# Kernel optimization log

Hardware: AMD Instinct MI355X
Metric: run time of the kernel (lower is better)

The kernel has to match this reference:

```python
import jax, jax.numpy as jnp
import numpy as np

CX, CY, FX, FY = 334.081, 169.808, 460.585, 460.268
EPS = 1e-07
T_ITER = 1000
MIN_POINTS = 5000
H, W, B = 360, 640, 2


def _point_cloud(depth_img):
    # depth_img: [C,H,W]; channel 2 if C==3 else channel 0
    depth = depth_img[2] if depth_img.shape[0] == 3 else depth_img[0]
    rows, cols = depth.shape
    c = jnp.arange(cols, dtype=depth.dtype)[None, :]
    r = jnp.arange(rows, dtype=depth.dtype)[:, None]
    valid = (depth > 0) & (depth < 65535)
    nanv = jnp.float32(jnp.nan)
    z = jnp.where(valid, depth / 1000.0, nanv)
    x = jnp.where(valid, z * (c - CX) / FX, nanv)
    y = jnp.where(valid, z * (r - CY) / FY, nanv)
    pcd = jnp.stack([x.ravel(), y.ravel(), z.ravel()], axis=1)  # [N,3]
    return pcd, valid.ravel()


def setup_inputs() -> dict:
    key = jax.random.key(0)
    k1, k2 = jax.random.split(key)
    fake = jax.random.uniform(k1, (B, 1, H, W), dtype=jnp.float32)
    real = jax.random.uniform(k2, (B, 1, H, W), dtype=jnp.float32)
    return {"fake": fake, "real": real, "epoch": 5, "show_image": 0}


def _forward(fake, real, epoch):
    real_pcd, vr = _point_cloud(real[0])
    fake_pcd, vf = _point_cloud(fake[0])
    real_pcd = real_pcd * 1000.0
    fake_pcd = fake_pcd * 1000.0
    # pcd[pcd==0] = eps  (NaN==0 is False, NaNs preserved)
    real_pcd = jnp.where(real_pcd == 0, EPS, real_pcd)
    fake_pcd = jnp.where(fake_pcd == 0, EPS, fake_pcd)

    # combined validity mask (real-valid then fake-valid filtering chain)
    m = vr & vf
    cnt = jnp.maximum(jnp.sum(m), 1)

    def sel(v, fill):
        return jnp.where(m, v, fill)

    def mrmse(a, b):
        d = sel(a, 0.0) - sel(b, 0.0)
        return jnp.sqrt(jnp.sum(d * d) / cnt)

    lossX = mrmse(real_pcd[:, 0], fake_pcd[:, 0])
    lossY = mrmse(real_pcd[:, 1], fake_pcd[:, 1])
    lossZ = mrmse(real_pcd[:, 2], fake_pcd[:, 2])
    dlog = jnp.log(jnp.abs(sel(real_pcd[:, 2], 1.0))) - jnp.log(jnp.abs(sel(fake_pcd[:, 2], 1.0)))
    RMSE_log = 10000.0 * jnp.sqrt(jnp.sum(jnp.where(m, dlog * dlog, 0.0)) / cnt)
    loss17 = RMSE_log * jnp.abs(10.0 * (3.0 - jnp.exp(lossX) - jnp.exp(lossY) - jnp.exp(lossZ)))

    # ---- batched RANSAC plane fit on normalized fake cloud ----
    nan_cloud = jnp.where(jnp.isnan(fake_pcd), 0.0, fake_pcd)
    pts = nan_cloud / jnp.max(nan_cloud)  # [N,3]
    N = pts.shape[0]
    thresh = jnp.maximum(jnp.float32(0.025 - 0.001 * epoch), jnp.float32(0.005))

    rkey = jax.random.key(42)
    idx = jax.random.randint(rkey, (T_ITER, 3), 0, N)  # 3 sample points per trial
    p = pts[idx]  # [T,3,3]
    vA = p[:, 1] - p[:, 0]
    vB = p[:, 2] - p[:, 0]
    nrm = jnp.cross(vA, vB)
    nrm = nrm / jnp.linalg.norm(nrm, axis=1, keepdims=True)  # unit normals [T,3]
    kk = -jnp.sum(nrm * p[:, 1], axis=1)  # plane offsets [T]
    dist = pts @ nrm.T + kk[None, :]  # [N,T], |n|=1 so no extra divide
    inl = jnp.abs(dist) <= thresh  # [N,T]
    counts = jnp.sum(inl, axis=0)  # [T]
    # keep first trial with strictly-largest count among counts > minPoints
    score = jnp.where(counts > MIN_POINTS, counts, -1)
    best = jnp.argmax(score)
    a, b, c, d = nrm[best, 0], nrm[best, 1], nrm[best, 2], kk[best]
    inlier_mask = inl[:, best]  # [N]

    # translation/rotation were built via torch.tensor(...) -> detached in torch
    trans = jax.lax.stop_gradient(jnp.stack([jnp.zeros(()), jnp.zeros(()), d / c]))
    n2 = a * a + b * b + c * c
    cos_t = c / jnp.sqrt(n2)
    sin_t = jnp.sqrt((a * a + b * b) / n2)
    sab = jnp.sqrt(a * a + b * b)
    u1 = b / sab
    u2 = -a / sab
    R = jnp.stack([
        jnp.stack([cos_t + u1 * u1 * (1 - cos_t), u1 * u2 * (1 - cos_t), u2 * sin_t]),
        jnp.stack([u1 * u2 * (1 - cos_t), cos_t + u2 * u2 * (1 - cos_t), -u1 * sin_t]),
        jnp.stack([-u2 * sin_t, u1 * sin_t, cos_t]),
    ])
    Rt = jax.lax.stop_gradient(R).T  # torch transposes before matmul

    plane_pts = pts + trans
    zc = (plane_pts @ Rt)[:, 2]  # rotated z for all points; inliers selected by mask
    icnt = jnp.maximum(jnp.sum(inlier_mask), 1)
    zmax = jnp.max(jnp.where(inlier_mask, zc, -jnp.inf))
    zmin = jnp.min(jnp.where(inlier_mask, zc, jnp.inf))
    below = jnp.sum(jnp.where(inlier_mask, jnp.abs(zc - zmax), 0.0)) / icnt
    above = jnp.sum(jnp.where(inlier_mask, jnp.abs(zc - zmin), 0.0)) / icnt
    above = jnp.where(above == 0, jnp.float32(1e-07), above)
    plane_mean_dist_grad = 1000.0 * (above + below)

    loss_curv = loss17 + plane_mean_dist_grad
    delta = jnp.stack([RMSE_log, lossX, lossY, lossZ, plane_mean_dist_grad, loss17])
    return delta, loss_curv


def reference(fake, real, epoch, show_image):
    del show_image  # unused in the loss math
    return _forward(fake, real, epoch)
```

## Files before the change

kernel.cpp:

```cpp
#include <hip/hip_runtime.h>

namespace {

typedef float v2f __attribute__((ext_vector_type(2)));

constexpr int kW = 640;
constexpr unsigned kSpan = 230400u;
constexpr int kB1 = 900;
constexpr int kB3 = 1800;
constexpr int kPPB3 = 128;
constexpr int kChunk = 113;
constexpr int kB5 = 900;

constexpr size_t kOffMaxv    = 0;
constexpr size_t kOffL17     = 8;
constexpr size_t kOffSel     = 16;
constexpr size_t kOffPlanes  = 512;
constexpr size_t kOffSP      = 512 + 16384;
constexpr size_t kOffZP      = 60416;
constexpr size_t kOffPartial = 90112;
constexpr size_t kOffPts     = 2097152;

__device__ __forceinline__ unsigned rotl32(unsigned v, int r) {
  return (v << r) | (v >> (32 - r));
}

__device__ __forceinline__ void threefry(unsigned c0, unsigned c1,
                                         unsigned& o0, unsigned& o1) {
  const unsigned ks0 = 0u, ks1 = 42u, ks2 = 0x1BD11BDAu ^ 0u ^ 42u;
  unsigned x0 = c0 + ks0, x1 = c1 + ks1;
#define TFR(r) { x0 += x1; x1 = rotl32(x1, (r)); x1 ^= x0; }
  TFR(13) TFR(15) TFR(26) TFR(6)
  x0 += ks1; x1 += ks2 + 1u;
  TFR(17) TFR(29) TFR(16) TFR(24)
  x0 += ks2; x1 += ks0 + 2u;
  TFR(13) TFR(15) TFR(26) TFR(6)
  x0 += ks0; x1 += ks1 + 3u;
  TFR(17) TFR(29) TFR(16) TFR(24)
  x0 += ks1; x1 += ks2 + 4u;
  TFR(13) TFR(15) TFR(26) TFR(6)
  x0 += ks2; x1 += ks0 + 5u;
#undef TFR
  o0 = x0; o1 = x1;
}

__device__ __forceinline__ void pix_coords(float d, int row, int col, bool& valid,
                                           float& x, float& y, float& z) {
  valid = (d > 0.0f) && (d < 65535.0f);
  float z0 = d / 1000.0f;
  float x0 = z0 * ((float)col - 334.081f) / 460.585f;
  float y0 = z0 * ((float)row - 169.808f) / 460.268f;
  x = x0 * 1000.0f;
  y = y0 * 1000.0f;
  z = z0 * 1000.0f;
  if (x == 0.0f) x = 1e-7f;
  if (y == 0.0f) y = 1e-7f;
  if (z == 0.0f) z = 1e-7f;
}

__device__ __forceinline__ void make_pt(float d, int row, int col, float maxv,
                                        float& x, float& y, float& z) {
  bool v; float a, b, c;
  pix_coords(d, row, col, v, a, b, c);
  x = (v ? a : 0.f) / maxv;
  y = (v ? b : 0.f) / maxv;
  z = (v ? c : 0.f) / maxv;
}

__device__ __forceinline__ float get_thresh(int ep) {
  return (float)fmax(0.025 - 0.001 * (double)ep, 0.005);
}

__global__ __launch_bounds__(256) void k_stats(const float* __restrict__ fake,
                                               const float* __restrict__ real,
                                               char* __restrict__ ws) {
  int* maxvBits = (int*)(ws + kOffMaxv);
  double* sp = (double*)(ws + kOffSP);
  float4* ptsraw = (float4*)(ws + kOffPts);

  const int b = blockIdx.x, t = threadIdx.x;
  const int lane = t & 63, wid = t >> 6;

  __shared__ double sD0[4], sD1[4], sD2[4], sD3[4];
  __shared__ int sI0[4];
  __shared__ float sF0[4];

  int i = b * 256 + t;
  int row = i / kW, col = i - row * kW;
  bool vr, vf; float rx, ry, rz, fx, fy, fz;
  pix_coords(real[i], row, col, vr, rx, ry, rz);
  pix_coords(fake[i], row, col, vf, fx, fy, fz);
  ptsraw[i] = make_float4(vf ? fx : 0.f, vf ? fy : 0.f, vf ? fz : 0.f, 0.f);
  double dx2 = 0, dy2 = 0, dz2 = 0, dl2 = 0; int cc = 0;
  if (vr && vf) {
    float ddx = rx - fx, ddy = ry - fy, ddz = rz - fz;
    dx2 = (double)ddx * (double)ddx;
    dy2 = (double)ddy * (double)ddy;
    dz2 = (double)ddz * (double)ddz;
    double dl = log(fabs((double)rz)) - log(fabs((double)fz));
    dl2 = dl * dl;
    cc = 1;
  }
  float mx = vf ? fmaxf(fmaxf(fx, fy), fz) : 0.0f;
  for (int o = 32; o; o >>= 1) {
    dx2 += __shfl_down(dx2, o); dy2 += __shfl_down(dy2, o);
    dz2 += __shfl_down(dz2, o); dl2 += __shfl_down(dl2, o);
    cc += __shfl_down(cc, o);
    mx = fmaxf(mx, __shfl_down(mx, o));
  }
  if (lane == 0) { sD0[wid]=dx2; sD1[wid]=dy2; sD2[wid]=dz2; sD3[wid]=dl2;
                   sI0[wid]=cc; sF0[wid]=mx; }
  __syncthreads();
  if (t == 0) {
    double* e = sp + (size_t)b * 6;
    e[0] = sD0[0]+sD0[1]+sD0[2]+sD0[3];
    e[1] = sD1[0]+sD1[1]+sD1[2]+sD1[3];
    e[2] = sD2[0]+sD2[1]+sD2[2]+sD2[3];
    e[3] = sD3[0]+sD3[1]+sD3[2]+sD3[3];
    e[4] = (double)(sI0[0]+sI0[1]+sI0[2]+sI0[3]);
    float bm = fmaxf(fmaxf(sF0[0], sF0[1]), fmaxf(sF0[2], sF0[3]));
    atomicMax(maxvBits, (int)__float_as_uint(bm));
  }
}

__global__ __launch_bounds__(256) void k_planes_scalars(const float* __restrict__ fake,
                                                        float* __restrict__ out,
                                                        char* __restrict__ ws) {
  const int* maxvBits = (const int*)(ws + kOffMaxv);
  double* loss17p = (double*)(ws + kOffL17);
  unsigned* selkeyp = (unsigned*)(ws + kOffSel);
  float4* planes = (float4*)(ws + kOffPlanes);
  const double* sp = (const double*)(ws + kOffSP);

  const int t = threadIdx.x;
  const int lane = t & 63, wid = t >> 6;

  if (blockIdx.x == 16) {
    __shared__ double sD0[4], sD1[4], sD2[4], sD3[4];
    __shared__ int sI0[4];
    double gx = 0, gy = 0, gz = 0, gl = 0; int gc = 0;
    for (int r = t; r < kB1; r += 256) {
      const double* e = sp + (size_t)r * 6;
      gx += e[0]; gy += e[1]; gz += e[2]; gl += e[3];
      gc += (int)e[4];
    }
    for (int o = 32; o; o >>= 1) {
      gx += __shfl_down(gx, o); gy += __shfl_down(gy, o);
      gz += __shfl_down(gz, o); gl += __shfl_down(gl, o);
      gc += __shfl_down(gc, o);
    }
    if (lane == 0) { sD0[wid]=gx; sD1[wid]=gy; sD2[wid]=gz; sD3[wid]=gl; sI0[wid]=gc; }
    __syncthreads();
    if (t == 0) {
      double SX = sD0[0]+sD0[1]+sD0[2]+sD0[3];
      double SY = sD1[0]+sD1[1]+sD1[2]+sD1[3];
      double SZ = sD2[0]+sD2[1]+sD2[2]+sD2[3];
      double SL = sD3[0]+sD3[1]+sD3[2]+sD3[3];
      int CN = sI0[0]+sI0[1]+sI0[2]+sI0[3];
      double cntd = (CN > 0) ? (double)CN : 1.0;
      double lossX = sqrt(SX / cntd);
      double lossY = sqrt(SY / cntd);
      double lossZ = sqrt(SZ / cntd);
      double rmse_log = 10000.0 * sqrt(SL / cntd);
      double loss17 = rmse_log * fabs(10.0 * (3.0 - exp(lossX) - exp(lossY) - exp(lossZ)));
      *loss17p = loss17;
      *selkeyp = 0u;
      out[0] = (float)rmse_log;
      out[1] = (float)lossX;
      out[2] = (float)lossY;
      out[3] = (float)lossZ;
      out[5] = (float)loss17;
    }
  } else {
    const float maxv = __uint_as_float((unsigned)*maxvBits);
    __shared__ float sX[192], sY[192], sZ[192];
    if (t < 192) {
      int j = t / 3;
      int v = t - j * 3;
      int pid = blockIdx.x * 64 + j;
      if (pid < 1000) {
        unsigned p = 3u * (unsigned)pid + (unsigned)v;
        unsigned o0, o1;
        threefry(p, p + 3000u, o0, o1);
        unsigned idx = o1 % kSpan;
        int row = (int)(idx / kW), col = (int)idx - row * kW;
        float x, y, z;
        make_pt(fake[idx], row, col, maxv, x, y, z);
        sX[t] = x; sY[t] = y; sZ[t] = z;
      }
    }
    __syncthreads();
    if (t < 64) {
      int pid = blockIdx.x * 64 + t;
      if (pid < 1000) {
        float px[3], py[3], pz[3];
#pragma unroll
        for (int v = 0; v < 3; v++) {
          px[v] = sX[3 * t + v]; py[v] = sY[3 * t + v]; pz[v] = sZ[3 * t + v];
        }
        float ax = px[1]-px[0], ay = py[1]-py[0], az = pz[1]-pz[0];
        float bx = px[2]-px[0], by = py[2]-py[0], bz = pz[2]-pz[0];
        float nx = ay*bz - az*by;
        float ny = az*bx - ax*bz;
        float nz = ax*by - ay*bx;
        float nn = sqrtf(nx*nx + ny*ny + nz*nz);
        nx /= nn; ny /= nn; nz /= nn;
        float kk = -(nx*px[1] + ny*py[1] + nz*pz[1]);
        planes[pid] = make_float4(nx, ny, nz, kk);
      } else {
        planes[pid] = make_float4(0.f, 0.f, 0.f, 3e38f);
      }
    }
  }
}

__global__ __launch_bounds__(256) void k_count(const int* __restrict__ epoch,
                                               char* __restrict__ ws) {
  const float4* planes = (const float4*)(ws + kOffPlanes);
  unsigned* partial = (unsigned*)(ws + kOffPartial);
  const float4* ptsraw = (const float4*)(ws + kOffPts);

  const int b = blockIdx.x, t = threadIdx.x;
  const float th = get_thresh(*epoch);
  const float maxv = __uint_as_float(*(const unsigned*)(ws + kOffMaxv));

  __shared__ float4 sPts[kPPB3];

  if (t < kPPB3) {
    float4 r = ptsraw[b * kPPB3 + t];
    sPts[t] = make_float4(r.x / maxv, r.y / maxv, r.z / maxv, 0.f);
  }
  float4 p0 = planes[t * 4 + 0], p1 = planes[t * 4 + 1];
  float4 p2 = planes[t * 4 + 2], p3 = planes[t * 4 + 3];
  v2f Ax = {p0.x, p1.x}, Ay = {p0.y, p1.y}, Az = {p0.z, p1.z}, Aw = {p0.w, p1.w};
  v2f Bx = {p2.x, p3.x}, By = {p2.y, p3.y}, Bz = {p2.z, p3.z}, Bw = {p2.w, p3.w};
  __syncthreads();

  int c0 = 0, c1 = 0, c2 = 0, c3 = 0;
#pragma unroll 4
  for (int s = 0; s < kPPB3; ++s) {
    float4 q = sPts[s];
    v2f qx = {q.x, q.x}, qy = {q.y, q.y}, qz = {q.z, q.z};
    v2f dA = __builtin_elementwise_fma(qx, Ax,
             __builtin_elementwise_fma(qy, Ay,
             __builtin_elementwise_fma(qz, Az, Aw)));
    v2f dB = __builtin_elementwise_fma(qx, Bx,
             __builtin_elementwise_fma(qy, By,
             __builtin_elementwise_fma(qz, Bz, Bw)));
    c0 += (fabsf(dA.x) <= th) ? 1 : 0;
    c1 += (fabsf(dA.y) <= th) ? 1 : 0;
    c2 += (fabsf(dB.x) <= th) ? 1 : 0;
    c3 += (fabsf(dB.y) <= th) ? 1 : 0;
  }
  partial[b * 256 + t] =
      (unsigned)c0 | ((unsigned)c1 << 8) | ((unsigned)c2 << 16) | ((unsigned)c3 << 24);
}

__global__ __launch_bounds__(256) void k_select(char* __restrict__ ws) {
  unsigned* selkeyp = (unsigned*)(ws + kOffSel);
  const unsigned* partial = (const unsigned*)(ws + kOffPartial);

  const int r = blockIdx.x;
  const int t = threadIdx.x;

  __shared__ uint4 sAcc[16][16];

  int owner = r * 16 + (t & 15);
  int chunk = t >> 4;
  int rbeg = chunk * kChunk;
  int rend = rbeg + kChunk; if (rend > kB3) rend = kB3;
  unsigned s0 = 0, s1 = 0, s2 = 0, s3 = 0;
  for (int row = rbeg; row < rend; ++row) {
    unsigned v = partial[row * 256 + owner];
    s0 += v & 0xFFu; s1 += (v >> 8) & 0xFFu;
    s2 += (v >> 16) & 0xFFu; s3 += (v >> 24) & 0xFFu;
  }
  sAcc[t & 15][chunk] = make_uint4(s0, s1, s2, s3);
  __syncthreads();

  unsigned mykey = 0u;
  if (t < 16) {
    unsigned t0 = 0, t1 = 0, t2 = 0, t3 = 0;
    for (int j = 0; j < 16; ++j) {
      uint4 v = sAcc[t][j];
      t0 += v.x; t1 += v.y; t2 += v.z; t3 += v.w;
    }
    unsigned tot[4] = {t0, t1, t2, t3};
    int pbase = (r * 16 + t) * 4;
#pragma unroll
    for (int k = 0; k < 4; ++k) {
      int p = pbase + k;
      if (p < 1000) {
        int score = ((int)tot[k] > 5000) ? (int)tot[k] : -1;
        unsigned key = ((unsigned)(score + 2) << 10) | (unsigned)(1023 - p);
        mykey = key > mykey ? key : mykey;
      }
    }
  }
  for (int o = 32; o; o >>= 1) {
    unsigned other = __shfl_down(mykey, o);
    mykey = other > mykey ? other : mykey;
  }
  if (t == 0) atomicMax(selkeyp, mykey);
}

__global__ __launch_bounds__(256) void k_zc(const int* __restrict__ epoch,
                                            char* __restrict__ ws) {
  const float4* planes = (const float4*)(ws + kOffPlanes);
  unsigned long long* zp = (unsigned long long*)(ws + kOffZP);
  const float4* ptsraw = (const float4*)(ws + kOffPts);

  const int b = blockIdx.x, t = threadIdx.x;
  const int lane = t & 63, wid = t >> 6;
  const float th = get_thresh(*epoch);
  const float maxv = __uint_as_float(*(const unsigned*)(ws + kOffMaxv));

  unsigned selkey = *(const unsigned*)(ws + kOffSel);
  int best = 1023 - (int)(selkey & 1023u);
  float4 pl = planes[best];
  const float a = pl.x, bb = pl.y, c = pl.z, d = pl.w;
  float n2 = a * a + bb * bb + c * c;
  float cos_t = c / sqrtf(n2);
  float sin_t = sqrtf((a * a + bb * bb) / n2);
  float sab = sqrtf(a * a + bb * bb);
  float u1 = bb / sab, u2 = -a / sab;
  const float r0 = -u2 * sin_t, r1 = u1 * sin_t, r2 = cos_t, tz = d / c;

  __shared__ double sD0[4];
  __shared__ int sI0[4];
  __shared__ float sF0[4], sF1[4];

  double sz = 0.0; int ic = 0; float zmx = -INFINITY, zmn = -INFINITY;
  {
    float4 rw = ptsraw[b * 256 + t];
    float qx = rw.x / maxv, qy = rw.y / maxv, qz = rw.z / maxv;
    float dist = fmaf(qx, a, fmaf(qy, bb, fmaf(qz, c, d)));
    if (fabsf(dist) <= th) {
      float zc = fmaf(qx, r0, fmaf(qy, r1, (qz + tz) * r2));
      sz = (double)zc; ic = 1; zmx = zc; zmn = -zc;
    }
  }
  for (int o = 32; o; o >>= 1) {
    sz += __shfl_down(sz, o); ic += __shfl_down(ic, o);
    zmx = fmaxf(zmx, __shfl_down(zmx, o));
    zmn = fmaxf(zmn, __shfl_down(zmn, o));
  }
  if (lane == 0) { sD0[wid] = sz; sI0[wid] = ic; sF0[wid] = zmx; sF1[wid] = zmn; }
  __syncthreads();
  if (t == 0) {
    unsigned long long* e = zp + (size_t)b * 4;
    e[0] = __double_as_longlong(sD0[0]+sD0[1]+sD0[2]+sD0[3]);
    e[1] = (unsigned long long)(sI0[0]+sI0[1]+sI0[2]+sI0[3]);
    float bmx = fmaxf(fmaxf(sF0[0], sF0[1]), fmaxf(sF0[2], sF0[3]));
    float bmn = fmaxf(fmaxf(sF1[0], sF1[1]), fmaxf(sF1[2], sF1[3]));
    e[2] = (unsigned long long)__float_as_uint(bmx) |
           ((unsigned long long)__float_as_uint(bmn) << 32);
  }
}

__global__ __launch_bounds__(256) void k_final(float* __restrict__ out,
                                               char* __restrict__ ws) {
  const double* loss17p = (const double*)(ws + kOffL17);
  const unsigned long long* zp = (const unsigned long long*)(ws + kOffZP);

  const int t = threadIdx.x;
  const int lane = t & 63, wid = t >> 6;

  __shared__ double sD0[4];
  __shared__ int sI0[4];
  __shared__ float sF0[4], sF1[4];

  double gs = 0.0; int gi = 0; float gmx = -INFINITY, gmn = -INFINITY;
  for (int r = t; r < kB5; r += 256) {
    const unsigned long long* e = zp + (size_t)r * 4;
    gs += __longlong_as_double(e[0]);
    gi += (int)e[1];
    unsigned long long mm = e[2];
    gmx = fmaxf(gmx, __uint_as_float((unsigned)(mm & 0xFFFFFFFFu)));
    gmn = fmaxf(gmn, __uint_as_float((unsigned)(mm >> 32)));
  }
  for (int o = 32; o; o >>= 1) {
    gs += __shfl_down(gs, o); gi += __shfl_down(gi, o);
    gmx = fmaxf(gmx, __shfl_down(gmx, o));
    gmn = fmaxf(gmn, __shfl_down(gmn, o));
  }
  if (lane == 0) { sD0[wid] = gs; sI0[wid] = gi; sF0[wid] = gmx; sF1[wid] = gmn; }
  __syncthreads();
  if (t == 0) {
    double S = sD0[0]+sD0[1]+sD0[2]+sD0[3];
    int IC = sI0[0]+sI0[1]+sI0[2]+sI0[3];
    float MX = fmaxf(fmaxf(sF0[0], sF0[1]), fmaxf(sF0[2], sF0[3]));
    float MN = fmaxf(fmaxf(sF1[0], sF1[1]), fmaxf(sF1[2], sF1[3]));
    double below = 0.0, above = 0.0;
    if (IC > 0) {
      double icd = (double)IC;
      double mean = S / icd;
      below = (double)MX - mean;
      above = mean - (double)(-MN);
    }
    if (above == 0.0) above = 1e-7;
    double pmdg = 1000.0 * (above + below);
    out[4] = (float)pmdg;
    out[6] = (float)(*loss17p + pmdg);
  }
}

}

extern "C" void kernel_launch(void* const* d_in, const int* in_sizes, int n_in,
                              void* d_out, int out_size, void* d_ws, size_t ws_size,
                              hipStream_t stream) {
  (void)in_sizes; (void)n_in; (void)out_size; (void)ws_size;
  const float* fake = (const float*)d_in[0];
  const float* real = (const float*)d_in[1];
  const int* epoch = (const int*)d_in[2];
  float* out = (float*)d_out;
  char* ws = (char*)d_ws;

  k_stats<<<kB1, 256, 0, stream>>>(fake, real, ws);
  k_planes_scalars<<<17, 256, 0, stream>>>(fake, out, ws);
  k_count<<<kB3, 256, 0, stream>>>(epoch, ws);
  k_select<<<16, 256, 0, stream>>>(ws);
  k_zc<<<kB5, 256, 0, stream>>>(epoch, ws);
  k_final<<<1, 256, 0, stream>>>(out, ws);
}
```

Baseline: 136.5 us.

## Prenormalize point cloud once and read points directly in count kernel

```diff
diff --git a/kernel.cpp b/kernel.cpp
--- a/kernel.cpp
+++ b/kernel.cpp
@@ -7,9 +7,8 @@
 constexpr int kW = 640;
 constexpr unsigned kSpan = 230400u;
 constexpr int kB1 = 900;
-constexpr int kB3 = 1800;
-constexpr int kPPB3 = 128;
-constexpr int kChunk = 113;
+constexpr int kB3 = 1024;
+constexpr int kPPB3 = 225;
 constexpr int kB5 = 900;
 
 constexpr size_t kOffMaxv    = 0;
@@ -17,8 +16,8 @@
 constexpr size_t kOffSel     = 16;
 constexpr size_t kOffPlanes  = 512;
 constexpr size_t kOffSP      = 512 + 16384;
-constexpr size_t kOffZP      = 60416;
-constexpr size_t kOffPartial = 90112;
+constexpr size_t kOffZP      = 61440;
+constexpr size_t kOffPartial = 98304;
 constexpr size_t kOffPts     = 2097152;
 
 __device__ __forceinline__ unsigned rotl32(unsigned v, int r) {
@@ -123,19 +122,25 @@
   }
 }
 
-__global__ __launch_bounds__(256) void k_planes_scalars(const float* __restrict__ fake,
-                                                        float* __restrict__ out,
-                                                        char* __restrict__ ws) {
+__global__ __launch_bounds__(256) void k_mid(const float* __restrict__ fake,
+                                             float* __restrict__ out,
+                                             char* __restrict__ ws) {
   const int* maxvBits = (const int*)(ws + kOffMaxv);
   double* loss17p = (double*)(ws + kOffL17);
   unsigned* selkeyp = (unsigned*)(ws + kOffSel);
   float4* planes = (float4*)(ws + kOffPlanes);
   const double* sp = (const double*)(ws + kOffSP);
+  float4* pts = (float4*)(ws + kOffPts);
 
   const int t = threadIdx.x;
   const int lane = t & 63, wid = t >> 6;
 
-  if (blockIdx.x == 16) {
+  if (blockIdx.x >= 17) {
+    const float maxv = __uint_as_float((unsigned)*maxvBits);
+    int i = (blockIdx.x - 17) * 256 + t;
+    float4 r = pts[i];
+    pts[i] = make_float4(r.x / maxv, r.y / maxv, r.z / maxv, 0.f);
+  } else if (blockIdx.x == 16) {
     __shared__ double sD0[4], sD1[4], sD2[4], sD3[4];
     __shared__ int sI0[4];
     double gx = 0, gy = 0, gz = 0, gl = 0; int gc = 0;
@@ -215,31 +220,23 @@
 }
 
 __global__ __launch_bounds__(256) void k_count(const int* __restrict__ epoch,
-                                               char* __restrict__ ws) {
-  const float4* planes = (const float4*)(ws + kOffPlanes);
-  unsigned* partial = (unsigned*)(ws + kOffPartial);
-  const float4* ptsraw = (const float4*)(ws + kOffPts);
-
+                                               const float4* __restrict__ planes,
+                                               const float4* __restrict__ pts,
+                                               unsigned* __restrict__ partial) {
   const int b = blockIdx.x, t = threadIdx.x;
   const float th = get_thresh(*epoch);
-  const float maxv = __uint_as_float(*(const unsigned*)(ws + kOffMaxv));
-
-  __shared__ float4 sPts[kPPB3];
-
-  if (t < kPPB3) {
-    float4 r = ptsraw[b * kPPB3 + t];
-    sPts[t] = make_float4(r.x / maxv, r.y / maxv, r.z / maxv, 0.f);
-  }
+
   float4 p0 = planes[t * 4 + 0], p1 = planes[t * 4 + 1];
   float4 p2 = planes[t * 4 + 2], p3 = planes[t * 4 + 3];
   v2f Ax = {p0.x, p1.x}, Ay = {p0.y, p1.y}, Az = {p0.z, p1.z}, Aw = {p0.w, p1.w};
   v2f Bx = {p2.x, p3.x}, By = {p2.y, p3.y}, Bz = {p2.z, p3.z}, Bw = {p2.w, p3.w};
-  __syncthreads();
+
+  const float4* __restrict__ base = pts + b * kPPB3;
 
   int c0 = 0, c1 = 0, c2 = 0, c3 = 0;
-#pragma unroll 4
+#pragma unroll 5
   for (int s = 0; s < kPPB3; ++s) {
-    float4 q = sPts[s];
+    float4 q = base[s];
     v2f qx = {q.x, q.x}, qy = {q.y, q.y}, qz = {q.z, q.z};
     v2f dA = __builtin_elementwise_fma(qx, Ax,
              __builtin_elementwise_fma(qy, Ay,
@@ -267,10 +264,8 @@
 
   int owner = r * 16 + (t & 15);
   int chunk = t >> 4;
-  int rbeg = chunk * kChunk;
-  int rend = rbeg + kChunk; if (rend > kB3) rend = kB3;
   unsigned s0 = 0, s1 = 0, s2 = 0, s3 = 0;
-  for (int row = rbeg; row < rend; ++row) {
+  for (int row = chunk * 64; row < chunk * 64 + 64; ++row) {
     unsigned v = partial[row * 256 + owner];
     s0 += v & 0xFFu; s1 += (v >> 8) & 0xFFu;
     s2 += (v >> 16) & 0xFFu; s3 += (v >> 24) & 0xFFu;
@@ -308,12 +303,11 @@
                                             char* __restrict__ ws) {
   const float4* planes = (const float4*)(ws + kOffPlanes);
   unsigned long long* zp = (unsigned long long*)(ws + kOffZP);
-  const float4* ptsraw = (const float4*)(ws + kOffPts);
+  const float4* pts = (const float4*)(ws + kOffPts);
 
   const int b = blockIdx.x, t = threadIdx.x;
   const int lane = t & 63, wid = t >> 6;
   const float th = get_thresh(*epoch);
-  const float maxv = __uint_as_float(*(const unsigned*)(ws + kOffMaxv));
 
   unsigned selkey = *(const unsigned*)(ws + kOffSel);
   int best = 1023 - (int)(selkey & 1023u);
@@ -332,11 +326,10 @@
 
   double sz = 0.0; int ic = 0; float zmx = -INFINITY, zmn = -INFINITY;
   {
-    float4 rw = ptsraw[b * 256 + t];
-    float qx = rw.x / maxv, qy = rw.y / maxv, qz = rw.z / maxv;
-    float dist = fmaf(qx, a, fmaf(qy, bb, fmaf(qz, c, d)));
+    float4 q = pts[b * 256 + t];
+    float dist = fmaf(q.x, a, fmaf(q.y, bb, fmaf(q.z, c, d)));
     if (fabsf(dist) <= th) {
-      float zc = fmaf(qx, r0, fmaf(qy, r1, (qz + tz) * r2));
+      float zc = fmaf(q.x, r0, fmaf(q.y, r1, (q.z + tz) * r2));
       sz = (double)zc; ic = 1; zmx = zc; zmn = -zc;
     }
   }
@@ -417,9 +410,13 @@
   float* out = (float*)d_out;
   char* ws = (char*)d_ws;
 
+  const float4* planes = (const float4*)(ws + kOffPlanes);
+  const float4* pts    = (const float4*)(ws + kOffPts);
+  unsigned* partial    = (unsigned*)(ws + kOffPartial);
+
   k_stats<<<kB1, 256, 0, stream>>>(fake, real, ws);
-  k_planes_scalars<<<17, 256, 0, stream>>>(fake, out, ws);
-  k_count<<<kB3, 256, 0, stream>>>(epoch, ws);
+  k_mid<<<917, 256, 0, stream>>>(fake, out, ws);
+  k_count<<<kB3, 256, 0, stream>>>(epoch, planes, pts, partial);
   k_select<<<16, 256, 0, stream>>>(ws);
   k_zc<<<kB5, 256, 0, stream>>>(epoch, ws);
   k_final<<<1, 256, 0, stream>>>(out, ws);
```

After: 125.4 us. -8.2%, faster.
